# Performance work log

Hardware: AMD Instinct MI355X
Metric: run time of the kernel (lower is better)

Reference implementation:

```python
import jax, jax.numpy as jnp
import numpy as np

N, D_MODEL, D_PE, H = 4096, 512, 16, 8


def setup_inputs() -> dict:
    key = jax.random.key(0)
    ks = jax.random.split(key, 6)
    s = 1.0 / np.sqrt(D_MODEL)
    return {
        "x": jax.random.normal(ks[0], (N, D_MODEL), dtype=jnp.float32),
        "pe": jax.random.normal(ks[1], (N, D_PE), dtype=jnp.float32),
        "w_qkv": jax.random.normal(ks[2], (D_MODEL, 3 * D_MODEL), dtype=jnp.float32) * s,
        "b_qkv": jnp.zeros((3 * D_MODEL,), dtype=jnp.float32),
        "w_pe": jax.random.normal(ks[3], (D_PE, H), dtype=jnp.float32) * (1.0 / np.sqrt(D_PE)),
        "b_pe": jnp.zeros((H,), dtype=jnp.float32),
        "w_out": jax.random.normal(ks[4], (D_MODEL, D_MODEL), dtype=jnp.float32) * s,
        "b_out": jnp.zeros((D_MODEL,), dtype=jnp.float32),
    }


def reference(x, pe, w_qkv, b_qkv, w_pe, b_pe, w_out, b_out):
    n, d = x.shape
    h = w_pe.shape[1]
    hd = d // h
    scale = hd ** -0.5

    qkv = (x @ w_qkv + b_qkv).reshape(n, 3, h, hd)  # [N,3,H,hd]
    q = jnp.transpose(qkv[:, 0], (1, 0, 2))  # [H,N,hd]
    k = jnp.transpose(qkv[:, 1], (1, 0, 2))
    v = jnp.transpose(qkv[:, 2], (1, 0, 2))

    pe_proj = pe @ w_pe + b_pe  # [N,H]
    # bias[h,i,j] = pe_proj[j,h] - pe_proj[i,h]  (matches torch unsqueeze/permute)
    pt = pe_proj.T  # [H,N]
    bias = pt[:, None, :] - pt[:, :, None]  # [H,N,N]

    scores = jnp.einsum('hnd,hmd->hnm', q, k) * scale + bias  # [H,N,N]
    attn = jax.nn.softmax(scores, axis=-1)
    out = jnp.einsum('hnm,hmd->hnd', attn, v)  # [H,N,hd]
    out = jnp.transpose(out, (1, 0, 2)).reshape(n, d)
    return out @ w_out + b_out
```

## Files before the change

kernel.cpp:

```cpp
#include <hip/hip_runtime.h>
#include <stdint.h>
#include <stddef.h>


typedef unsigned short u16;
typedef __attribute__((ext_vector_type(8))) short short8;
typedef __attribute__((ext_vector_type(8))) unsigned short us8;
typedef __attribute__((ext_vector_type(4))) unsigned short us4;
typedef __attribute__((ext_vector_type(4))) float floatx4;

__device__ __forceinline__ u16 f2b(float f) {
  union { float f; uint32_t u; } v; v.f = f;
  uint32_t u = v.u;
  return (u16)((u + 0x7fffu + ((u >> 16) & 1u)) >> 16);
}

__device__ __forceinline__ uint32_t pkbf16(float a, float b) {
  union { float f; uint32_t u; } x, y; x.f = a; y.f = b;
  return __builtin_amdgcn_perm(y.u + 0x8000u, x.u + 0x8000u, 0x07060302u);
}

#if __has_builtin(__builtin_amdgcn_exp2f)
__device__ __forceinline__ float fexp2(float x) { return __builtin_amdgcn_exp2f(x); }
#else
__device__ __forceinline__ float fexp2(float x) { return exp2f(x); }
#endif

__device__ __forceinline__ void gld16(const u16* g, u16* l) {
  __builtin_amdgcn_global_load_lds(
      (const __attribute__((address_space(1))) uint32_t*)(const void*)g,
      (__attribute__((address_space(3))) uint32_t*)(void*)l, 16, 0, 0);
}


__device__ __forceinline__ void tr_tile(const float* __restrict__ in,
                                        u16* __restrict__ out, int R, int C,
                                        int bx, int by, u16 (*tile)[33]) {
  int tx = threadIdx.x & 31, ty = threadIdx.x >> 5;
  int c0 = bx * 32, r0 = by * 32;
#pragma unroll
  for (int i = 0; i < 32; i += 8)
    tile[ty + i][tx] = f2b(in[(size_t)(r0 + ty + i) * C + c0 + tx]);
  __syncthreads();
#pragma unroll
  for (int i = 0; i < 32; i += 8)
    out[(size_t)(c0 + ty + i) * R + r0 + tx] = tile[tx][ty + i];
}

__global__ __launch_bounds__(256) void k_prep(
    const float* __restrict__ x, u16* __restrict__ xb,
    const float* __restrict__ w_qkv, u16* __restrict__ wqkvT,
    const float* __restrict__ w_out, u16* __restrict__ woutT,
    const float* __restrict__ pe, const float* __restrict__ w_pe,
    const float* __restrict__ b_pe, float* __restrict__ wexp,
    u16* __restrict__ wpb) {
  __shared__ u16 tile[32][33];
  int b = blockIdx.x;
  if (b < 2048) {
    int i = b * 256 + threadIdx.x;
    float4 v = ((const float4*)x)[i];
    uint2 o = make_uint2(pkbf16(v.x, v.y), pkbf16(v.z, v.w));
    ((uint2*)xb)[i] = o;
  } else if (b < 2816) {
    int idx = b - 2048;
    tr_tile(w_qkv, wqkvT, 512, 1536, idx % 48, idx / 48, tile);
  } else if (b < 3072) {
    int idx = b - 2816;
    tr_tile(w_out, woutT, 512, 512, idx % 16, idx / 16, tile);
  } else {
    int idx = (b - 3072) * 256 + threadIdx.x;
    int h = idx >> 12, n = idx & 4095;
    float acc = b_pe[h];
#pragma unroll
    for (int d = 0; d < 16; ++d) acc = fmaf(pe[n * 16 + d], w_pe[d * 8 + h], acc);
    float w = exp2f(acc * 1.4426950408889634f - 16.0f);
    u16 wb = f2b(w);
    union { uint32_t u; float f; } cv; cv.u = ((uint32_t)wb) << 16;
    wexp[h * 4096 + n] = cv.f;
    int pn = (n & ~31) | (((n >> 2) & 3) << 3) | (((n >> 4) & 1) << 2) | (n & 3);
    wpb[h * 4096 + pn] = wb;
  }
}


__global__ __launch_bounds__(512, 6) void k_gemm_qkv(const u16* __restrict__ A,
                                                     const u16* __restrict__ Bt,
                                                     const float* __restrict__ bias,
                                                     const float* __restrict__ wexp,
                                                     u16* __restrict__ qk,
                                                     u16* __restrict__ vtp) {
  __shared__ __align__(16) u16 smem[24576];
  const int tid = threadIdx.x;
  const int lane = tid & 63, wave = tid >> 6;
  const int colx = lane & 15, quad = lane >> 4;
  const int m0 = blockIdx.y * 64, n0 = blockIdx.x * 128;
  const int wm = wave >> 2, wn = wave & 3;
  const int sc = (lane & 7) ^ ((lane >> 3) & 7);
  const floatx4 fz = {0.f, 0.f, 0.f, 0.f};
  floatx4 acc[2][2];
#pragma unroll
  for (int i = 0; i < 2; ++i)
#pragma unroll
    for (int j = 0; j < 2; ++j) acc[i][j] = fz;

#define PREF_QKV(k0, b)                                                       \
  {                                                                           \
    int rowa = wave * 8 + (lane >> 3);                                        \
    gld16(&A[(size_t)(m0 + rowa) * 512 + (k0) + sc * 8],                      \
          &smem[(b) * 4096 + wave * 512 + lane * 8]);                         \
    _Pragma("unroll") for (int c = 0; c < 2; ++c) {                           \
      int rowb = wave * 16 + c * 8 + (lane >> 3);                             \
      gld16(&Bt[(size_t)(n0 + rowb) * 512 + (k0) + sc * 8],                   \
            &smem[8192 + (b) * 8192 + wave * 1024 + c * 512 + lane * 8]);     \
    }                                                                         \
  }

  PREF_QKV(0, 0);
  __syncthreads();
  for (int it = 0; it < 8; ++it) {
    int cur = it & 1;
    if (it < 7) PREF_QKV((it + 1) * 64, cur ^ 1);
    const u16* As = &smem[cur * 4096];
    const u16* Bs = &smem[8192 + cur * 8192];
#pragma unroll
    for (int kk = 0; kk < 2; ++kk) {
      short8 af[2], bf[2];
#pragma unroll
      for (int i = 0; i < 2; ++i) {
        int row = wm * 32 + i * 16 + colx;
        af[i] = *(const short8*)&As[row * 64 + (((kk * 4 + quad) ^ (colx & 7))) * 8];
      }
#pragma unroll
      for (int j = 0; j < 2; ++j) {
        int row = wn * 32 + j * 16 + colx;
        bf[j] = *(const short8*)&Bs[row * 64 + (((kk * 4 + quad) ^ (colx & 7))) * 8];
      }
#pragma unroll
      for (int i = 0; i < 2; ++i)
#pragma unroll
        for (int j = 0; j < 2; ++j)
          acc[i][j] = __builtin_amdgcn_mfma_f32_16x16x32_bf16(af[i], bf[j], acc[i][j], 0, 0, 0);
    }
    __syncthreads();
  }

  const bool isV = (blockIdx.x >= 8);
  if (!isV) {
#pragma unroll
    for (int j = 0; j < 2; ++j) {
      int c = n0 + wn * 32 + j * 16 + colx;
      float bq = bias[c];
      float qs = (c < 512) ? 0.18033688011112042f : 1.0f;
#pragma unroll
      for (int i = 0; i < 2; ++i)
#pragma unroll
        for (int r = 0; r < 4; ++r) {
          int row = m0 + wm * 32 + i * 16 + quad * 4 + r;
          qk[(size_t)row * 1024 + c] = f2b((acc[i][j][r] + bq) * qs);
        }
    }
  } else {
    const int dv = n0 - 1024;
    u16* Vl = smem;
    const int hh = (dv + wn * 32) >> 6;
#pragma unroll
    for (int j = 0; j < 2; ++j) {
      float bq = bias[n0 + wn * 32 + j * 16 + colx];
#pragma unroll
      for (int i = 0; i < 2; ++i) {
        floatx4 wv = *(const floatx4*)&wexp[hh * 4096 + m0 + wm * 32 + i * 16 + quad * 4];
        us4 o;
#pragma unroll
        for (int r = 0; r < 4; ++r) o[r] = f2b((acc[i][j][r] + bq) * wv[r]);
        int dl = wn * 32 + j * 16 + colx;
        int nc = wm * 32 + quad * 8 + i * 4;
        *(us4*)&Vl[dl * 72 + nc] = o;
      }
    }
    __syncthreads();
#pragma unroll
    for (int t = 0; t < 2; ++t) {
      int idx = t * 512 + tid;
      int dl = idx >> 3, ch = idx & 7;
      *(us8*)&vtp[(size_t)(dv + dl) * 4096 + m0 + ch * 8] =
          *(const us8*)&Vl[dl * 72 + ch * 8];
    }
  }
#undef PREF_QKV
}


__global__ __launch_bounds__(256, 4) void k_flash(const u16* __restrict__ qk,
                                                  const u16* __restrict__ vt,
                                                  const u16* __restrict__ wpb,
                                                  u16* __restrict__ ao) {
  __shared__ __align__(16) u16 smem[20480];
  float* bufs = (float*)smem;

  const int tid = threadIdx.x;
  const int lane = tid & 63, wave = tid >> 6;
  const int colx = lane & 15, quad = lane >> 4;
  const int ih = wave >> 1, jq = wave & 1;
  const int q0 = blockIdx.x * 64;
  const int h = blockIdx.y;
  const floatx4 fz = {0.f, 0.f, 0.f, 0.f};

  const int sc = (lane & 7) ^ ((lane >> 3) & 7);
  const int srow = wave * 16 + (lane >> 3);

#pragma unroll
  for (int t = 0; t < 2; ++t) {
    int idx = t * 256 + tid;
    int row = idx >> 3, ch = idx & 7;
    *(us8*)&smem[row * 64 + (ch ^ (row & 7)) * 8] =
        *(const us8*)&qk[(size_t)(q0 + row) * 1024 + h * 64 + ch * 8];
  }
  const u16* qptr = qk + (size_t)srow * 1024 + 512 + h * 64 + sc * 8;
  const u16* vptr = vt + (size_t)(h * 64 + srow) * 4096 + sc * 8;
  const u16* wptr = wpb + h * 4096 + jq * 32 + quad * 8;
  gld16(qptr, &smem[4096 + wave * 1024 + lane * 8]);
  gld16(qptr + 8192, &smem[4096 + wave * 1024 + 512 + lane * 8]);
  gld16(vptr, &smem[12288 + wave * 1024 + lane * 8]);
  gld16(vptr + 32768, &smem[12288 + wave * 1024 + 512 + lane * 8]);
  qptr += 65536;
  vptr += 64;
  __syncthreads();

  short8 qf[2][2];
#pragma unroll
  for (int iq = 0; iq < 2; ++iq)
#pragma unroll
    for (int kk = 0; kk < 2; ++kk) {
      int row = ih * 32 + iq * 16 + colx;
      qf[iq][kk] = *(const short8*)&smem[row * 64 + (((kk * 4 + quad) ^ (colx & 7))) * 8];
    }

  floatx4 oacc[2][4], lacc[2];
  lacc[0] = fz; lacc[1] = fz;
#pragma unroll
  for (int iq = 0; iq < 2; ++iq)
#pragma unroll
    for (int cb = 0; cb < 4; ++cb) oacc[iq][cb] = fz;

#define FBODY(CUR, PREF)                                                      \
  {                                                                           \
    short8 wf = *(const short8*)wptr;                                         \
    wptr += 64;                                                               \
    if (PREF) {                                                               \
      gld16(qptr, &smem[4096 + (1 - (CUR)) * 4096 + wave * 1024 + lane * 8]); \
      gld16(qptr + 8192,                                                      \
            &smem[4096 + (1 - (CUR)) * 4096 + wave * 1024 + 512 + lane * 8]); \
      gld16(vptr, &smem[12288 + (1 - (CUR)) * 4096 + wave * 1024 + lane * 8]);\
      gld16(vptr + 32768,                                                     \
            &smem[12288 + (1 - (CUR)) * 4096 + wave * 1024 + 512 + lane * 8]);\
      qptr += 65536;                                                          \
      vptr += 64;                                                             \
    }                                                                         \
    const u16* Ks = &smem[4096 + (CUR) * 4096];                               \
    const u16* Vts = &smem[12288 + (CUR) * 4096];                             \
    floatx4 sacc[2][2] = {{fz, fz}, {fz, fz}};                                \
    _Pragma("unroll") for (int j2 = 0; j2 < 2; ++j2) {                        \
      _Pragma("unroll") for (int kk = 0; kk < 2; ++kk) {                      \
        int row = jq * 32 + j2 * 16 + colx;                                   \
        short8 kf = *(const short8*)&Ks[row * 64 +                            \
                                        (((kk * 4 + quad) ^ (colx & 7))) * 8];\
        sacc[0][j2] = __builtin_amdgcn_mfma_f32_16x16x32_bf16(                \
            kf, qf[0][kk], sacc[0][j2], 0, 0, 0);                             \
        sacc[1][j2] = __builtin_amdgcn_mfma_f32_16x16x32_bf16(                \
            kf, qf[1][kk], sacc[1][j2], 0, 0, 0);                             \
      }                                                                       \
    }                                                                         \
    union { uint32_t w[4]; short8 s; } pk[2];                                 \
    _Pragma("unroll") for (int iq = 0; iq < 2; ++iq) {                        \
      _Pragma("unroll") for (int j2 = 0; j2 < 2; ++j2) {                      \
        float p0 = fexp2(sacc[iq][j2][0]);                                    \
        float p1 = fexp2(sacc[iq][j2][1]);                                    \
        float p2 = fexp2(sacc[iq][j2][2]);                                    \
        float p3 = fexp2(sacc[iq][j2][3]);                                    \
        pk[iq].w[j2 * 2 + 0] = pkbf16(p0, p1);                                \
        pk[iq].w[j2 * 2 + 1] = pkbf16(p2, p3);                                \
      }                                                                       \
    }                                                                         \
    _Pragma("unroll") for (int cb = 0; cb < 4; ++cb) {                        \
      int row = cb * 16 + colx;                                               \
      short8 vf = *(const short8*)&Vts[row * 64 +                             \
                                       (((jq * 4 + quad) ^ (colx & 7))) * 8]; \
      oacc[0][cb] = __builtin_amdgcn_mfma_f32_16x16x32_bf16(                  \
          pk[0].s, vf, oacc[0][cb], 0, 0, 0);                                 \
      oacc[1][cb] = __builtin_amdgcn_mfma_f32_16x16x32_bf16(                  \
          pk[1].s, vf, oacc[1][cb], 0, 0, 0);                                 \
    }                                                                         \
    lacc[0] = __builtin_amdgcn_mfma_f32_16x16x32_bf16(pk[0].s, wf, lacc[0], 0, 0, 0); \
    lacc[1] = __builtin_amdgcn_mfma_f32_16x16x32_bf16(pk[1].s, wf, lacc[1], 0, 0, 0); \
    __syncthreads();                                                          \
  }

  for (int t = 0; t < 31; ++t) {
    FBODY(0, 1)
    FBODY(1, 1)
  }
  FBODY(0, 1)
  FBODY(1, 0)
#undef FBODY

  float* b = bufs + ih * 2080;
  if (jq == 1) {
#pragma unroll
    for (int iq = 0; iq < 2; ++iq)
#pragma unroll
      for (int cb = 0; cb < 4; ++cb)
#pragma unroll
        for (int r = 0; r < 4; ++r)
          b[(iq * 16 + quad * 4 + r) * 65 + cb * 16 + colx] = oacc[iq][cb][r];
    if (colx == 0)
#pragma unroll
      for (int iq = 0; iq < 2; ++iq)
#pragma unroll
        for (int r = 0; r < 4; ++r) b[(iq * 16 + quad * 4 + r) * 65 + 64] = lacc[iq][r];
  }
  __syncthreads();
  if (jq == 0) {
#pragma unroll
    for (int iq = 0; iq < 2; ++iq) {
#pragma unroll
      for (int cb = 0; cb < 4; ++cb)
#pragma unroll
        for (int r = 0; r < 4; ++r)
          oacc[iq][cb][r] += b[(iq * 16 + quad * 4 + r) * 65 + cb * 16 + colx];
#pragma unroll
      for (int r = 0; r < 4; ++r) lacc[iq][r] += b[(iq * 16 + quad * 4 + r) * 65 + 64];
    }
#pragma unroll
    for (int iq = 0; iq < 2; ++iq) {
      float inv[4];
#pragma unroll
      for (int r = 0; r < 4; ++r) inv[r] = 1.0f / lacc[iq][r];
#pragma unroll
      for (int cb = 0; cb < 4; ++cb)
#pragma unroll
        for (int r = 0; r < 4; ++r) {
          int row = q0 + ih * 32 + iq * 16 + quad * 4 + r;
          ao[(size_t)row * 512 + h * 64 + cb * 16 + colx] =
              f2b(oacc[iq][cb][r] * inv[r]);
        }
    }
  }
}


__global__ __launch_bounds__(512, 4) void k_gemm_out(const u16* __restrict__ A,
                                                     const u16* __restrict__ Bt,
                                                     const float* __restrict__ bias,
                                                     float* __restrict__ Cout) {
  __shared__ __align__(16) u16 smem[16384];
  const int tid = threadIdx.x;
  const int lane = tid & 63, wave = tid >> 6;
  const int colx = lane & 15, quad = lane >> 4;
  const int m0 = blockIdx.y * 64, n0 = blockIdx.x * 64;
  const int wm = wave >> 2, wn = wave & 3;
  const int sc = (lane & 7) ^ ((lane >> 3) & 7);
  const floatx4 fz = {0.f, 0.f, 0.f, 0.f};
  floatx4 acc[2];
  acc[0] = fz; acc[1] = fz;

#define PREF_OUT(k0, b)                                                       \
  {                                                                           \
    int rowa = wave * 8 + (lane >> 3);                                        \
    gld16(&A[(size_t)(m0 + rowa) * 512 + (k0) + sc * 8],                      \
          &smem[(b) * 4096 + wave * 512 + lane * 8]);                         \
    gld16(&Bt[(size_t)(n0 + rowa) * 512 + (k0) + sc * 8],                     \
          &smem[8192 + (b) * 4096 + wave * 512 + lane * 8]);                  \
  }

  PREF_OUT(0, 0);
  __syncthreads();
  for (int it = 0; it < 8; ++it) {
    int cur = it & 1;
    if (it < 7) PREF_OUT((it + 1) * 64, cur ^ 1);
    const u16* As = &smem[cur * 4096];
    const u16* Bs = &smem[8192 + cur * 4096];
#pragma unroll
    for (int kk = 0; kk < 2; ++kk) {
      short8 af[2], bf;
#pragma unroll
      for (int i = 0; i < 2; ++i) {
        int row = wm * 32 + i * 16 + colx;
        af[i] = *(const short8*)&As[row * 64 + (((kk * 4 + quad) ^ (colx & 7))) * 8];
      }
      {
        int row = wn * 16 + colx;
        bf = *(const short8*)&Bs[row * 64 + (((kk * 4 + quad) ^ (colx & 7))) * 8];
      }
#pragma unroll
      for (int i = 0; i < 2; ++i)
        acc[i] = __builtin_amdgcn_mfma_f32_16x16x32_bf16(af[i], bf, acc[i], 0, 0, 0);
    }
    __syncthreads();
  }
  int c = n0 + wn * 16 + colx;
  float bq = bias[c];
#pragma unroll
  for (int i = 0; i < 2; ++i)
#pragma unroll
    for (int r = 0; r < 4; ++r) {
      int row = m0 + wm * 32 + i * 16 + quad * 4 + r;
      Cout[(size_t)row * 512 + c] = acc[i][r] + bq;
    }
#undef PREF_OUT
}


extern "C" void kernel_launch(void* const* d_in, const int* in_sizes, int n_in,
                              void* d_out, int out_size, void* d_ws, size_t ws_size,
                              hipStream_t stream) {
  const float* x     = (const float*)d_in[0];
  const float* pe    = (const float*)d_in[1];
  const float* w_qkv = (const float*)d_in[2];
  const float* b_qkv = (const float*)d_in[3];
  const float* w_pe  = (const float*)d_in[4];
  const float* b_pe  = (const float*)d_in[5];
  const float* w_out = (const float*)d_in[6];
  const float* b_out = (const float*)d_in[7];
  float* out = (float*)d_out;

  u16* xb    = (u16*)d_ws;
  u16* wqkvT = xb    + 2097152;
  u16* woutT = wqkvT + 786432;
  u16* qk    = woutT + 262144;
  u16* vt    = qk    + 4194304;
  u16* wpb   = vt    + 2097152;
  u16* ao    = wpb   + 32768;
  float* wexp  = (float*)(ao + 2097152);

  k_prep<<<3200, 256, 0, stream>>>(x, xb, w_qkv, wqkvT, w_out, woutT,
                                   pe, w_pe, b_pe, wexp, wpb);
  k_gemm_qkv<<<dim3(12, 64), 512, 0, stream>>>(xb, wqkvT, b_qkv, wexp, qk, vt);
  k_flash<<<dim3(64, 8), 256, 0, stream>>>(qk, vt, wpb, ao);
  k_gemm_out<<<dim3(8, 64), 512, 0, stream>>>(ao, woutT, b_out, out);
}
```

Before: 137.7 us.

## Split flash attention KV range across two wave groups per block

Doubles the flash kernel block to 512 threads, with two wave groups that each handle half of the key/value sequence using separate double-buffered shared-memory regions. Their partial outputs and row sums are merged through shared memory at the end. The grid stays at 512 blocks but has twice the waves, which gives more latency hiding per CU. It also adds s_setprio around the MFMA sections. The cost is larger LDS use per block and an extra reduction step, which may limit how many blocks fit on a CU.

Result: no change. 139.1 us (+1.0%).

```diff
diff --git a/kernel.cpp b/kernel.cpp
--- a/kernel.cpp
+++ b/kernel.cpp
@@ -190,38 +190,39 @@
 }
 
 
-__global__ __launch_bounds__(256, 4) void k_flash(const u16* __restrict__ qk,
+__global__ __launch_bounds__(512, 4) void k_flash(const u16* __restrict__ qk,
                                                   const u16* __restrict__ vt,
                                                   const u16* __restrict__ wpb,
                                                   u16* __restrict__ ao) {
-  __shared__ __align__(16) u16 smem[20480];
+  __shared__ __align__(16) u16 smem[36864];
   float* bufs = (float*)smem;
 
   const int tid = threadIdx.x;
   const int lane = tid & 63, wave = tid >> 6;
   const int colx = lane & 15, quad = lane >> 4;
-  const int ih = wave >> 1, jq = wave & 1;
+  const int zg = wave >> 2;
+  const int ih = (wave >> 1) & 1, jq = wave & 1;
+  const int gw = wave & 3;
   const int q0 = blockIdx.x * 64;
   const int h = blockIdx.y;
+  const int kvb = zg * 2048;
   const floatx4 fz = {0.f, 0.f, 0.f, 0.f};
 
   const int sc = (lane & 7) ^ ((lane >> 3) & 7);
-  const int srow = wave * 16 + (lane >> 3);
-
-#pragma unroll
-  for (int t = 0; t < 2; ++t) {
-    int idx = t * 256 + tid;
-    int row = idx >> 3, ch = idx & 7;
+  const int srow = gw * 16 + (lane >> 3);
+
+  {
+    int row = tid >> 3, ch = tid & 7;
     *(us8*)&smem[row * 64 + (ch ^ (row & 7)) * 8] =
         *(const us8*)&qk[(size_t)(q0 + row) * 1024 + h * 64 + ch * 8];
   }
-  const u16* qptr = qk + (size_t)srow * 1024 + 512 + h * 64 + sc * 8;
-  const u16* vptr = vt + (size_t)(h * 64 + srow) * 4096 + sc * 8;
-  const u16* wptr = wpb + h * 4096 + jq * 32 + quad * 8;
-  gld16(qptr, &smem[4096 + wave * 1024 + lane * 8]);
-  gld16(qptr + 8192, &smem[4096 + wave * 1024 + 512 + lane * 8]);
-  gld16(vptr, &smem[12288 + wave * 1024 + lane * 8]);
-  gld16(vptr + 32768, &smem[12288 + wave * 1024 + 512 + lane * 8]);
+  const u16* qptr = qk + (size_t)(kvb + srow) * 1024 + 512 + h * 64 + sc * 8;
+  const u16* vptr = vt + (size_t)(h * 64 + srow) * 4096 + kvb + sc * 8;
+  const u16* wptr = wpb + h * 4096 + kvb + jq * 32 + quad * 8;
+  gld16(qptr, &smem[4096 + (zg * 2) * 4096 + gw * 1024 + lane * 8]);
+  gld16(qptr + 8192, &smem[4096 + (zg * 2) * 4096 + gw * 1024 + 512 + lane * 8]);
+  gld16(vptr, &smem[20480 + (zg * 2) * 4096 + gw * 1024 + lane * 8]);
+  gld16(vptr + 32768, &smem[20480 + (zg * 2) * 4096 + gw * 1024 + 512 + lane * 8]);
   qptr += 65536;
   vptr += 64;
   __syncthreads();
@@ -247,18 +248,19 @@
     short8 wf = *(const short8*)wptr;                                         \
     wptr += 64;                                                               \
     if (PREF) {                                                               \
-      gld16(qptr, &smem[4096 + (1 - (CUR)) * 4096 + wave * 1024 + lane * 8]); \
+      gld16(qptr, &smem[4096 + (zg * 2 + 1 - (CUR)) * 4096 + gw * 1024 + lane * 8]); \
       gld16(qptr + 8192,                                                      \
-            &smem[4096 + (1 - (CUR)) * 4096 + wave * 1024 + 512 + lane * 8]); \
-      gld16(vptr, &smem[12288 + (1 - (CUR)) * 4096 + wave * 1024 + lane * 8]);\
+            &smem[4096 + (zg * 2 + 1 - (CUR)) * 4096 + gw * 1024 + 512 + lane * 8]); \
+      gld16(vptr, &smem[20480 + (zg * 2 + 1 - (CUR)) * 4096 + gw * 1024 + lane * 8]); \
       gld16(vptr + 32768,                                                     \
-            &smem[12288 + (1 - (CUR)) * 4096 + wave * 1024 + 512 + lane * 8]);\
+            &smem[20480 + (zg * 2 + 1 - (CUR)) * 4096 + gw * 1024 + 512 + lane * 8]); \
       qptr += 65536;                                                          \
       vptr += 64;                                                             \
     }                                                                         \
-    const u16* Ks = &smem[4096 + (CUR) * 4096];                               \
-    const u16* Vts = &smem[12288 + (CUR) * 4096];                             \
+    const u16* Ks = &smem[4096 + (zg * 2 + (CUR)) * 4096];                    \
+    const u16* Vts = &smem[20480 + (zg * 2 + (CUR)) * 4096];                  \
     floatx4 sacc[2][2] = {{fz, fz}, {fz, fz}};                                \
+    __builtin_amdgcn_s_setprio(1);                                            \
     _Pragma("unroll") for (int j2 = 0; j2 < 2; ++j2) {                        \
       _Pragma("unroll") for (int kk = 0; kk < 2; ++kk) {                      \
         int row = jq * 32 + j2 * 16 + colx;                                   \
@@ -270,6 +272,7 @@
             kf, qf[1][kk], sacc[1][j2], 0, 0, 0);                             \
       }                                                                       \
     }                                                                         \
+    __builtin_amdgcn_s_setprio(0);                                            \
     union { uint32_t w[4]; short8 s; } pk[2];                                 \
     _Pragma("unroll") for (int iq = 0; iq < 2; ++iq) {                        \
       _Pragma("unroll") for (int j2 = 0; j2 < 2; ++j2) {                      \
@@ -281,6 +284,7 @@
         pk[iq].w[j2 * 2 + 1] = pkbf16(p2, p3);                                \
       }                                                                       \
     }                                                                         \
+    __builtin_amdgcn_s_setprio(1);                                            \
     _Pragma("unroll") for (int cb = 0; cb < 4; ++cb) {                        \
       int row = cb * 16 + colx;                                               \
       short8 vf = *(const short8*)&Vts[row * 64 +                             \
@@ -292,10 +296,11 @@
     }                                                                         \
     lacc[0] = __builtin_amdgcn_mfma_f32_16x16x32_bf16(pk[0].s, wf, lacc[0], 0, 0, 0); \
     lacc[1] = __builtin_amdgcn_mfma_f32_16x16x32_bf16(pk[1].s, wf, lacc[1], 0, 0, 0); \
+    __builtin_amdgcn_s_setprio(0);                                            \
     __syncthreads();                                                          \
   }
 
-  for (int t = 0; t < 31; ++t) {
+  for (int t = 0; t < 15; ++t) {
     FBODY(0, 1)
     FBODY(1, 1)
   }
@@ -303,7 +308,7 @@
   FBODY(1, 0)
 #undef FBODY
 
-  float* b = bufs + ih * 2080;
+  float* b1 = bufs + (zg * 2 + ih) * 2080;
   if (jq == 1) {
 #pragma unroll
     for (int iq = 0; iq < 2; ++iq)
@@ -311,12 +316,12 @@
       for (int cb = 0; cb < 4; ++cb)
 #pragma unroll
         for (int r = 0; r < 4; ++r)
-          b[(iq * 16 + quad * 4 + r) * 65 + cb * 16 + colx] = oacc[iq][cb][r];
+          b1[(iq * 16 + quad * 4 + r) * 65 + cb * 16 + colx] = oacc[iq][cb][r];
     if (colx == 0)
 #pragma unroll
       for (int iq = 0; iq < 2; ++iq)
 #pragma unroll
-        for (int r = 0; r < 4; ++r) b[(iq * 16 + quad * 4 + r) * 65 + 64] = lacc[iq][r];
+        for (int r = 0; r < 4; ++r) b1[(iq * 16 + quad * 4 + r) * 65 + 64] = lacc[iq][r];
   }
   __syncthreads();
   if (jq == 0) {
@@ -326,9 +331,38 @@
       for (int cb = 0; cb < 4; ++cb)
 #pragma unroll
         for (int r = 0; r < 4; ++r)
-          oacc[iq][cb][r] += b[(iq * 16 + quad * 4 + r) * 65 + cb * 16 + colx];
-#pragma unroll
-      for (int r = 0; r < 4; ++r) lacc[iq][r] += b[(iq * 16 + quad * 4 + r) * 65 + 64];
+          oacc[iq][cb][r] += b1[(iq * 16 + quad * 4 + r) * 65 + cb * 16 + colx];
+#pragma unroll
+      for (int r = 0; r < 4; ++r) lacc[iq][r] += b1[(iq * 16 + quad * 4 + r) * 65 + 64];
+    }
+  }
+  __syncthreads();
+  float* b2 = bufs + ih * 2080;
+  if (zg == 1 && jq == 0) {
+#pragma unroll
+    for (int iq = 0; iq < 2; ++iq)
+#pragma unroll
+      for (int cb = 0; cb < 4; ++cb)
+#pragma unroll
+        for (int r = 0; r < 4; ++r)
+          b2[(iq * 16 + quad * 4 + r) * 65 + cb * 16 + colx] = oacc[iq][cb][r];
+    if (colx == 0)
+#pragma unroll
+      for (int iq = 0; iq < 2; ++iq)
+#pragma unroll
+        for (int r = 0; r < 4; ++r) b2[(iq * 16 + quad * 4 + r) * 65 + 64] = lacc[iq][r];
+  }
+  __syncthreads();
+  if (zg == 0 && jq == 0) {
+#pragma unroll
+    for (int iq = 0; iq < 2; ++iq) {
+#pragma unroll
+      for (int cb = 0; cb < 4; ++cb)
+#pragma unroll
+        for (int r = 0; r < 4; ++r)
+          oacc[iq][cb][r] += b2[(iq * 16 + quad * 4 + r) * 65 + cb * 16 + colx];
+#pragma unroll
+      for (int r = 0; r < 4; ++r) lacc[iq][r] += b2[(iq * 16 + quad * 4 + r) * 65 + 64];
     }
 #pragma unroll
     for (int iq = 0; iq < 2; ++iq) {
@@ -435,6 +469,6 @@
   k_prep<<<3200, 256, 0, stream>>>(x, xb, w_qkv, wqkvT, w_out, woutT,
                                    pe, w_pe, b_pe, wexp, wpb);
   k_gemm_qkv<<<dim3(12, 64), 512, 0, stream>>>(xb, wqkvT, b_qkv, wexp, qk, vt);
-  k_flash<<<dim3(64, 8), 256, 0, stream>>>(qk, vt, wpb, ao);
+  k_flash<<<dim3(64, 8), 512, 0, stream>>>(qk, vt, wpb, ao);
   k_gemm_out<<<dim3(8, 64), 512, 0, stream>>>(ao, woutT, b_out, out);
 }
```
